# Performance work log

Hardware: AMD Instinct MI355X
Metric: run time of the kernel (lower is better)

Reference implementation:

```python
import jax, jax.numpy as jnp
import numpy as np

PI = float(np.pi)

def erp_xyz_coords(h, w):
    # matches calculate_erp_coord: pixel grid -> uv -> unit-sphere xyz
    yy, xx = jnp.meshgrid(jnp.linspace(0.0, h - 1.0, h), jnp.linspace(0.0, w - 1.0, w), indexing='ij')
    u = (xx - (w / 2.0 + 0.5)) / w * 2.0 * PI
    v = (yy - (h / 2.0 + 0.5)) / h * PI
    xyz = jnp.stack([jnp.cos(v) * jnp.sin(u), jnp.sin(v), jnp.cos(v) * jnp.cos(u)], axis=-1)
    return xyz.reshape(h * w, 3)  # (HW, 3)


def setup_inputs() -> dict:
    key = jax.random.key(0)
    ks = jax.random.split(key, 16)
    B, C, H, W = 1, 128, 16, 32
    Nkv = 1280
    s = 0.02
    inp = {
        'erp_feature': jax.random.normal(ks[0], (B, C, H, W), jnp.float32),
        'ico_feature': jax.random.normal(ks[1], (B, Nkv, C), jnp.float32),
        'ico_coord': jax.random.normal(ks[2], (B, Nkv, 3), jnp.float32),
        # SA branch params (torch Linear: y = x @ W.T + b, W is (out,in))
        'Wq_sa': jax.random.normal(ks[3], (C, C), jnp.float32) * s,
        'Wkv_sa': jax.random.normal(ks[4], (2 * C, C), jnp.float32) * s,
        'proj_sa_w': jax.random.normal(ks[5], (C, C), jnp.float32) * s,
        'proj_sa_b': jnp.zeros((C,), jnp.float32),
        # DA branch params
        'Wq_da': jax.random.normal(ks[6], (C, C), jnp.float32) * s,
        'Wkv_da': jax.random.normal(ks[7], (2 * C, C), jnp.float32) * s,
        'Wdelta': jax.random.normal(ks[8], (C, 3), jnp.float32) * s,
        'proj_da_w': jax.random.normal(ks[9], (C, C), jnp.float32) * s,
        'proj_da_b': jnp.zeros((C,), jnp.float32),
        # gates
        'gate_sa_w': jax.random.normal(ks[10], (C, 2 * C), jnp.float32) * s,
        'gate_da_w': jax.random.normal(ks[11], (C, 2 * C), jnp.float32) * s,
    }
    return inp


def _forward(erp_feature, ico_feature, ico_coord,
             Wq_sa, Wkv_sa, proj_sa_w, proj_sa_b,
             Wq_da, Wkv_da, Wdelta, proj_da_w, proj_da_b,
             gate_sa_w, gate_da_w):
    B, C, H, W = erp_feature.shape
    Nq = H * W
    q = erp_feature.reshape(B, C, Nq).transpose(0, 2, 1)  # (B, Nq, C)
    qc = erp_xyz_coords(H, W)[None]                        # (1, Nq, 3) broadcasts over B

    # ---- SA branch (iteration = 1) ----
    q_sa = q @ Wq_sa.T                                     # (B, Nq, C)
    kv_sa = (ico_feature @ Wkv_sa.T).reshape(B, -1, 2, C)
    k_sa, v_sa = kv_sa[:, :, 0], kv_sa[:, :, 1]
    attn_sa = jax.nn.softmax(jnp.einsum('bqc,bkc->bqk', q_sa, k_sa) * (C ** -0.5), axis=-1)
    out_sa = jnp.einsum('bqk,bkc->bqc', attn_sa, v_sa)
    # faithful to torch: .transpose(1,2).reshape(B, Nq, C) scrambles layout
    out_sa = out_sa.transpose(0, 2, 1).reshape(B, Nq, C)
    sa = out_sa @ proj_sa_w.T + proj_sa_b

    # ---- DA branch (iteration = 1) ----
    q_da = q @ Wq_da.T
    kv_da = (ico_feature @ Wkv_da.T).reshape(B, -1, 2, C)
    k_da, v_da = kv_da[:, :, 0], kv_da[:, :, 1]
    # feature affinity: sum_c exp(-|q_c - k_c|)   -> (B, Nq, Nkv)
    feat_aff = jnp.exp(-jnp.abs(q_da[:, :, None, :] - k_da[:, None, :, :])).sum(-1)
    # positional term: (exp(-|dq - dk|) @ Wdelta.T).sum(-1) == exp(...) . Wdelta.sum(0)
    pos_exp = jnp.exp(-jnp.abs(qc[:, :, None, :] - ico_coord[:, None, :, :]))  # (B,Nq,Nkv,3)
    pos_aff = jnp.einsum('bqkt,t->bqk', pos_exp, Wdelta.sum(0))
    attn_da = jax.nn.softmax((feat_aff + pos_aff) * (1.0 / C), axis=-1)
    out_da = jnp.einsum('bqk,bkc->bqc', attn_da, v_da)
    da = out_da @ proj_da_w.T + proj_da_b

    # ---- gated fusion ----
    cat = jnp.concatenate([sa, da], axis=-1)               # (B, Nq, 2C)
    sa_factor = jax.nn.sigmoid(cat @ gate_sa_w.T)
    da_factor = jax.nn.sigmoid(cat @ gate_da_w.T)
    fused = sa_factor * sa + da_factor * da                # (B, Nq, C)
    return fused.reshape(B, H, W, C).transpose(0, 3, 1, 2)  # (B, C, H, W)


def reference(erp_feature, ico_feature, ico_coord,
              Wq_sa, Wkv_sa, proj_sa_w, proj_sa_b,
              Wq_da, Wkv_da, Wdelta, proj_da_w, proj_da_b,
              gate_sa_w, gate_da_w):
    return _forward(erp_feature, ico_feature, ico_coord,
                    Wq_sa, Wkv_sa, proj_sa_w, proj_sa_b,
                    Wq_da, Wkv_da, Wdelta, proj_da_w, proj_da_b,
                    gate_sa_w, gate_da_w)
```

## Files before the change

### kernel.cpp

```cpp
#include <hip/hip_runtime.h>
#include <math.h>

#define NQ   512
#define NKV  1280
#define CDIM 128

#define OFF_WDSUM 0
#define OFF_SUMS  16
#define OFF_QSA   1056
#define OFF_QDA   66592
#define OFF_KSAT  132128
#define OFF_VSA   295968
#define OFF_KDAT  459808
#define OFF_VDA   623648
#define OFF_OUT   787488

__global__ __launch_bounds__(256) void prep_kernel(
    const float* __restrict__ erp, const float* __restrict__ ico,
    const float* __restrict__ wq_sa, const float* __restrict__ wq_da,
    const float* __restrict__ wkv_sa, const float* __restrict__ wkv_da,
    const float* __restrict__ wdelta, float* __restrict__ ws)
{
  int bx = blockIdx.x, t = threadIdx.x;
  if (bx < 320) {
    __shared__ float x4[4 * CDIM];
    int k0 = bx * 4;
    for (int i = t; i < 512; i += 256) {
      int ky = i >> 7, j = i & 127;
      x4[j * 4 + ky] = ico[(k0 + ky) * CDIM + j];
    }
    __syncthreads();
    const float4* wsa4 = (const float4*)(wkv_sa + t * CDIM);
    const float4* wda4 = (const float4*)(wkv_da + t * CDIM);
    float as0=0,as1=0,as2=0,as3=0, ad0=0,ad1=0,ad2=0,ad3=0;
    #pragma unroll 4
    for (int j4 = 0; j4 < 32; ++j4) {
      float4 wsv = wsa4[j4];
      float4 wdv = wda4[j4];
      float4 x0 = *(const float4*)&x4[(j4 * 4 + 0) * 4];
      float4 x1 = *(const float4*)&x4[(j4 * 4 + 1) * 4];
      float4 x2 = *(const float4*)&x4[(j4 * 4 + 2) * 4];
      float4 x3 = *(const float4*)&x4[(j4 * 4 + 3) * 4];
      as0 = fmaf(wsv.x, x0.x, as0); as1 = fmaf(wsv.x, x0.y, as1);
      as2 = fmaf(wsv.x, x0.z, as2); as3 = fmaf(wsv.x, x0.w, as3);
      ad0 = fmaf(wdv.x, x0.x, ad0); ad1 = fmaf(wdv.x, x0.y, ad1);
      ad2 = fmaf(wdv.x, x0.z, ad2); ad3 = fmaf(wdv.x, x0.w, ad3);
      as0 = fmaf(wsv.y, x1.x, as0); as1 = fmaf(wsv.y, x1.y, as1);
      as2 = fmaf(wsv.y, x1.z, as2); as3 = fmaf(wsv.y, x1.w, as3);
      ad0 = fmaf(wdv.y, x1.x, ad0); ad1 = fmaf(wdv.y, x1.y, ad1);
      ad2 = fmaf(wdv.y, x1.z, ad2); ad3 = fmaf(wdv.y, x1.w, ad3);
      as0 = fmaf(wsv.z, x2.x, as0); as1 = fmaf(wsv.z, x2.y, as1);
      as2 = fmaf(wsv.z, x2.z, as2); as3 = fmaf(wsv.z, x2.w, as3);
      ad0 = fmaf(wdv.z, x2.x, ad0); ad1 = fmaf(wdv.z, x2.y, ad1);
      ad2 = fmaf(wdv.z, x2.z, ad2); ad3 = fmaf(wdv.z, x2.w, ad3);
      as0 = fmaf(wsv.w, x3.x, as0); as1 = fmaf(wsv.w, x3.y, as1);
      as2 = fmaf(wsv.w, x3.z, as2); as3 = fmaf(wsv.w, x3.w, as3);
      ad0 = fmaf(wdv.w, x3.x, ad0); ad1 = fmaf(wdv.w, x3.y, ad1);
      ad2 = fmaf(wdv.w, x3.z, ad2); ad3 = fmaf(wdv.w, x3.w, ad3);
    }
    if (t < 128) {
      *(float4*)(ws + OFF_KSAT + t * NKV + k0) = make_float4(as0, as1, as2, as3);
      *(float4*)(ws + OFF_KDAT + t * NKV + k0) = make_float4(ad0, ad1, ad2, ad3);
    } else {
      int c = t - 128;
      ws[OFF_VSA + (k0 + 0) * CDIM + c] = as0;
      ws[OFF_VSA + (k0 + 1) * CDIM + c] = as1;
      ws[OFF_VSA + (k0 + 2) * CDIM + c] = as2;
      ws[OFF_VSA + (k0 + 3) * CDIM + c] = as3;
      ws[OFF_VDA + (k0 + 0) * CDIM + c] = ad0;
      ws[OFF_VDA + (k0 + 1) * CDIM + c] = ad1;
      ws[OFF_VDA + (k0 + 2) * CDIM + c] = ad2;
      ws[OFF_VDA + (k0 + 3) * CDIM + c] = ad3;
    }
  } else if (bx < 448) {
    __shared__ float q4[4 * CDIM];
    int n0 = (bx - 320) * 4;
    for (int i = t; i < 512; i += 256)
      q4[i] = erp[(i >> 2) * NQ + n0 + (i & 3)];
    __syncthreads();
    const float* w = (t < 128) ? wq_sa : wq_da;
    int c = t & 127;
    const float4* w4 = (const float4*)(w + c * CDIM);
    float a0 = 0.f, a1 = 0.f, a2 = 0.f, a3 = 0.f;
    #pragma unroll 8
    for (int j4 = 0; j4 < 32; ++j4) {
      float4 wv = w4[j4];
      float4 q0 = *(const float4*)&q4[(j4 * 4 + 0) * 4];
      float4 q1 = *(const float4*)&q4[(j4 * 4 + 1) * 4];
      float4 q2 = *(const float4*)&q4[(j4 * 4 + 2) * 4];
      float4 q3 = *(const float4*)&q4[(j4 * 4 + 3) * 4];
      a0 = fmaf(wv.x, q0.x, a0); a1 = fmaf(wv.x, q0.y, a1);
      a2 = fmaf(wv.x, q0.z, a2); a3 = fmaf(wv.x, q0.w, a3);
      a0 = fmaf(wv.y, q1.x, a0); a1 = fmaf(wv.y, q1.y, a1);
      a2 = fmaf(wv.y, q1.z, a2); a3 = fmaf(wv.y, q1.w, a3);
      a0 = fmaf(wv.z, q2.x, a0); a1 = fmaf(wv.z, q2.y, a1);
      a2 = fmaf(wv.z, q2.z, a2); a3 = fmaf(wv.z, q2.w, a3);
      a0 = fmaf(wv.w, q3.x, a0); a1 = fmaf(wv.w, q3.y, a1);
      a2 = fmaf(wv.w, q3.z, a2); a3 = fmaf(wv.w, q3.w, a3);
    }
    float* o = ws + ((t < 128) ? OFF_QSA : OFF_QDA);
    o[(n0 + 0) * CDIM + c] = a0;
    o[(n0 + 1) * CDIM + c] = a1;
    o[(n0 + 2) * CDIM + c] = a2;
    o[(n0 + 3) * CDIM + c] = a3;
  } else if (bx == 448) {
    *(float4*)(ws + OFF_SUMS + t * 4) = make_float4(0.f, 0.f, 0.f, 0.f);
    if (t < 3) {
      float s = 0.f;
      for (int i = 0; i < 128; ++i) s += wdelta[i * 3 + t];
      ws[OFF_WDSUM + t] = s;
    }
  } else {
    int base = OFF_OUT + (bx - 449) * 1024 + t * 4;
    *(float4*)(ws + base) = make_float4(0.f, 0.f, 0.f, 0.f);
  }
}

__global__ __launch_bounds__(256) void attn_kernel(
    const float* __restrict__ coord, float* __restrict__ ws)
{
  __shared__ __align__(16) float qjf[128][4];
  __shared__ __align__(16) float se[4][256];
  __shared__ float red[4][4];
  __shared__ float qcr[4][3];
  __shared__ float wdl[3];
  int b = blockIdx.x, t = threadIdx.x;
  int br = (b < 1280) ? 1 : 0;
  int n0, k0;
  if (br) { int g = b / 10;          n0 = g * 4; k0 = (b - g * 10) * 128; }
  else    { int bb = b - 1280, g = bb / 5; n0 = g * 4; k0 = (bb - g * 5) * 256; }

  const float* qsrc = ws + (br ? OFF_QDA : OFF_QSA);
  for (int i = t; i < 512; i += 256)
    qjf[i >> 2][i & 3] = qsrc[(n0 + (i & 3)) * CDIM + (i >> 2)];
  if (br) {
    if (t < 4) {
      int n = n0 + t;
      float x = (float)(n & 31), y = (float)(n >> 5);
      float u  = (x - 16.5f) * 0.19634954084936207f;
      float vv = (y -  8.5f) * 0.19634954084936207f;
      float cv = cosf(vv);
      qcr[t][0] = cv * sinf(u);
      qcr[t][1] = sinf(vv);
      qcr[t][2] = cv * cosf(u);
    }
    if (t >= 64 && t < 67) wdl[t - 64] = ws[OFF_WDSUM + (t - 64)];
  }
  __syncthreads();

  if (br) {
    int kl = t & 127, rp = t >> 7;
    int k = k0 + kl, rp2 = rp * 2;
    float c0 = coord[3 * k], c1 = coord[3 * k + 1], c2 = coord[3 * k + 2];
    float w0 = wdl[0], w1 = wdl[1], w2 = wdl[2];
    float pA = w0 * __expf(-fabsf(qcr[rp2][0] - c0))
             + w1 * __expf(-fabsf(qcr[rp2][1] - c1))
             + w2 * __expf(-fabsf(qcr[rp2][2] - c2));
    float pB = w0 * __expf(-fabsf(qcr[rp2 + 1][0] - c0))
             + w1 * __expf(-fabsf(qcr[rp2 + 1][1] - c1))
             + w2 * __expf(-fabsf(qcr[rp2 + 1][2] - c2));
    const float* kt = ws + OFF_KDAT + k;
    float accA = 0.f, accB = 0.f;
    for (int j8 = 0; j8 < 128; j8 += 8) {
      float kv0 = kt[(j8 + 0) * NKV];
      float kv1 = kt[(j8 + 1) * NKV];
      float kv2 = kt[(j8 + 2) * NKV];
      float kv3 = kt[(j8 + 3) * NKV];
      float kv4 = kt[(j8 + 4) * NKV];
      float kv5 = kt[(j8 + 5) * NKV];
      float kv6 = kt[(j8 + 6) * NKV];
      float kv7 = kt[(j8 + 7) * NKV];
      float2 q0 = *(const float2*)&qjf[j8 + 0][rp2];
      float2 q1 = *(const float2*)&qjf[j8 + 1][rp2];
      float2 q2 = *(const float2*)&qjf[j8 + 2][rp2];
      float2 q3 = *(const float2*)&qjf[j8 + 3][rp2];
      float2 q4 = *(const float2*)&qjf[j8 + 4][rp2];
      float2 q5 = *(const float2*)&qjf[j8 + 5][rp2];
      float2 q6 = *(const float2*)&qjf[j8 + 6][rp2];
      float2 q7 = *(const float2*)&qjf[j8 + 7][rp2];
      accA += __expf(-fabsf(q0.x - kv0)); accB += __expf(-fabsf(q0.y - kv0));
      accA += __expf(-fabsf(q1.x - kv1)); accB += __expf(-fabsf(q1.y - kv1));
      accA += __expf(-fabsf(q2.x - kv2)); accB += __expf(-fabsf(q2.y - kv2));
      accA += __expf(-fabsf(q3.x - kv3)); accB += __expf(-fabsf(q3.y - kv3));
      accA += __expf(-fabsf(q4.x - kv4)); accB += __expf(-fabsf(q4.y - kv4));
      accA += __expf(-fabsf(q5.x - kv5)); accB += __expf(-fabsf(q5.y - kv5));
      accA += __expf(-fabsf(q6.x - kv6)); accB += __expf(-fabsf(q6.y - kv6));
      accA += __expf(-fabsf(q7.x - kv7)); accB += __expf(-fabsf(q7.y - kv7));
    }
    const float i128 = 0.0078125f;
    float eA = __expf((accA + pA) * i128);
    float eB = __expf((accB + pB) * i128);
    se[rp2][kl]     = eA;
    se[rp2 + 1][kl] = eB;
    float sA = eA, sB = eB;
    #pragma unroll
    for (int o = 32; o > 0; o >>= 1) {
      sA += __shfl_down(sA, o, 64); sB += __shfl_down(sB, o, 64);
    }
    if ((t & 63) == 0) { int w = t >> 6; red[w][0] = sA; red[w][1] = sB; }
    __syncthreads();
    if (t < 4) {
      int base = 2 * (t >> 1);
      atomicAdd(ws + OFF_SUMS + 512 + n0 + t,
                red[base][t & 1] + red[base + 1][t & 1]);
    }
    int c = t & 127, h = t >> 7;
    int kb = h * 64;
    const float* vp = ws + OFF_VDA + (k0 + kb) * CDIM + c;
    float a0 = 0.f, a1 = 0.f, a2 = 0.f, a3 = 0.f;
    #pragma unroll 2
    for (int ko = 0; ko < 64; ko += 4) {
      int kk = kb + ko;
      float4 p0 = *(const float4*)&se[0][kk];
      float4 p1 = *(const float4*)&se[1][kk];
      float4 p2 = *(const float4*)&se[2][kk];
      float4 p3 = *(const float4*)&se[3][kk];
      float v0 = vp[(ko + 0) * CDIM];
      float v1 = vp[(ko + 1) * CDIM];
      float v2 = vp[(ko + 2) * CDIM];
      float v3 = vp[(ko + 3) * CDIM];
      a0 = fmaf(p0.x, v0, a0); a0 = fmaf(p0.y, v1, a0);
      a0 = fmaf(p0.z, v2, a0); a0 = fmaf(p0.w, v3, a0);
      a1 = fmaf(p1.x, v0, a1); a1 = fmaf(p1.y, v1, a1);
      a1 = fmaf(p1.z, v2, a1); a1 = fmaf(p1.w, v3, a1);
      a2 = fmaf(p2.x, v0, a2); a2 = fmaf(p2.y, v1, a2);
      a2 = fmaf(p2.z, v2, a2); a2 = fmaf(p2.w, v3, a2);
      a3 = fmaf(p3.x, v0, a3); a3 = fmaf(p3.y, v1, a3);
      a3 = fmaf(p3.z, v2, a3); a3 = fmaf(p3.w, v3, a3);
    }
    float* op = ws + OFF_OUT + NQ * CDIM + c;
    atomicAdd(op + (n0 + 0) * CDIM, a0);
    atomicAdd(op + (n0 + 1) * CDIM, a1);
    atomicAdd(op + (n0 + 2) * CDIM, a2);
    atomicAdd(op + (n0 + 3) * CDIM, a3);
  } else {
    const float* kt = ws + OFF_KSAT + k0 + t;
    float acc0 = 0.f, acc1 = 0.f, acc2 = 0.f, acc3 = 0.f;
    for (int j4 = 0; j4 < 128; j4 += 4) {
      float kv0 = kt[(j4 + 0) * NKV];
      float kv1 = kt[(j4 + 1) * NKV];
      float kv2 = kt[(j4 + 2) * NKV];
      float kv3 = kt[(j4 + 3) * NKV];
      float4 q0 = *(const float4*)qjf[j4 + 0];
      float4 q1 = *(const float4*)qjf[j4 + 1];
      float4 q2 = *(const float4*)qjf[j4 + 2];
      float4 q3 = *(const float4*)qjf[j4 + 3];
      acc0 = fmaf(q0.x, kv0, acc0); acc1 = fmaf(q0.y, kv0, acc1);
      acc2 = fmaf(q0.z, kv0, acc2); acc3 = fmaf(q0.w, kv0, acc3);
      acc0 = fmaf(q1.x, kv1, acc0); acc1 = fmaf(q1.y, kv1, acc1);
      acc2 = fmaf(q1.z, kv1, acc2); acc3 = fmaf(q1.w, kv1, acc3);
      acc0 = fmaf(q2.x, kv2, acc0); acc1 = fmaf(q2.y, kv2, acc1);
      acc2 = fmaf(q2.z, kv2, acc2); acc3 = fmaf(q2.w, kv2, acc3);
      acc0 = fmaf(q3.x, kv3, acc0); acc1 = fmaf(q3.y, kv3, acc1);
      acc2 = fmaf(q3.z, kv3, acc2); acc3 = fmaf(q3.w, kv3, acc3);
    }
    const float scl = 0.088388347648318447f;
    float e0 = __expf(acc0 * scl);
    float e1 = __expf(acc1 * scl);
    float e2 = __expf(acc2 * scl);
    float e3 = __expf(acc3 * scl);
    se[0][t] = e0; se[1][t] = e1; se[2][t] = e2; se[3][t] = e3;
    float s0 = e0, s1 = e1, s2 = e2, s3 = e3;
    #pragma unroll
    for (int o = 32; o > 0; o >>= 1) {
      s0 += __shfl_down(s0, o, 64); s1 += __shfl_down(s1, o, 64);
      s2 += __shfl_down(s2, o, 64); s3 += __shfl_down(s3, o, 64);
    }
    if ((t & 63) == 0) {
      int w = t >> 6;
      red[w][0] = s0; red[w][1] = s1; red[w][2] = s2; red[w][3] = s3;
    }
    __syncthreads();
    if (t < 4)
      atomicAdd(ws + OFF_SUMS + n0 + t,
                red[0][t] + red[1][t] + red[2][t] + red[3][t]);
    int c = t & 127, h = t >> 7;
    int kb = h * 128;
    const float* vp = ws + OFF_VSA + (k0 + kb) * CDIM + c;
    float a0 = 0.f, a1 = 0.f, a2 = 0.f, a3 = 0.f;
    #pragma unroll 2
    for (int ko = 0; ko < 128; ko += 4) {
      int kk = kb + ko;
      float4 p0 = *(const float4*)&se[0][kk];
      float4 p1 = *(const float4*)&se[1][kk];
      float4 p2 = *(const float4*)&se[2][kk];
      float4 p3 = *(const float4*)&se[3][kk];
      float v0 = vp[(ko + 0) * CDIM];
      float v1 = vp[(ko + 1) * CDIM];
      float v2 = vp[(ko + 2) * CDIM];
      float v3 = vp[(ko + 3) * CDIM];
      a0 = fmaf(p0.x, v0, a0); a0 = fmaf(p0.y, v1, a0);
      a0 = fmaf(p0.z, v2, a0); a0 = fmaf(p0.w, v3, a0);
      a1 = fmaf(p1.x, v0, a1); a1 = fmaf(p1.y, v1, a1);
      a1 = fmaf(p1.z, v2, a1); a1 = fmaf(p1.w, v3, a1);
      a2 = fmaf(p2.x, v0, a2); a2 = fmaf(p2.y, v1, a2);
      a2 = fmaf(p2.z, v2, a2); a2 = fmaf(p2.w, v3, a2);
      a3 = fmaf(p3.x, v0, a3); a3 = fmaf(p3.y, v1, a3);
      a3 = fmaf(p3.z, v2, a3); a3 = fmaf(p3.w, v3, a3);
    }
    float* op = ws + OFF_OUT + c;
    atomicAdd(op + (n0 + 0) * CDIM, a0);
    atomicAdd(op + (n0 + 1) * CDIM, a1);
    atomicAdd(op + (n0 + 2) * CDIM, a2);
    atomicAdd(op + (n0 + 3) * CDIM, a3);
  }
}

__global__ __launch_bounds__(256) void finalize_kernel(
    const float* __restrict__ psa, const float* __restrict__ bsa,
    const float* __restrict__ pda, const float* __restrict__ bda,
    const float* __restrict__ gsa, const float* __restrict__ gda,
    float* __restrict__ out, float* __restrict__ ws)
{
  __shared__ float sain[2][CDIM];
  __shared__ float dain[2][CDIM];
  __shared__ float cat[2][2 * CDIM];
  __shared__ float gl[2][2][CDIM];
  int i0 = blockIdx.x * 2, t = threadIdx.x;
  int h = t >> 7, c = t & 127;
  #pragma unroll
  for (int rr = 0; rr < 2; ++rr) {
    int i = i0 + rr;
    if (h == 0) {
      int row = (i & 3) * 128 + c;
      float s = ws[OFF_SUMS + row];
      sain[rr][c] = ws[OFF_OUT + row * CDIM + (i >> 2)] / s;
    } else {
      float s = ws[OFF_SUMS + 512 + i];
      dain[rr][c] = ws[OFF_OUT + NQ * CDIM + i * CDIM + c] / s;
    }
  }
  __syncthreads();
  {
    const float4* w4 = (const float4*)((h ? pda : psa) + c * CDIM);
    const float* in0 = h ? dain[0] : sain[0];
    const float* in1 = h ? dain[1] : sain[1];
    float a0 = 0, a1 = 0, b0 = 0, b1 = 0;
    #pragma unroll 8
    for (int j4 = 0; j4 < 32; ++j4) {
      float4 wv = w4[j4];
      float4 x0 = *(const float4*)&in0[j4 * 4];
      float4 x1 = *(const float4*)&in1[j4 * 4];
      a0 = fmaf(wv.x, x0.x, a0); a1 = fmaf(wv.y, x0.y, a1);
      a0 = fmaf(wv.z, x0.z, a0); a1 = fmaf(wv.w, x0.w, a1);
      b0 = fmaf(wv.x, x1.x, b0); b1 = fmaf(wv.y, x1.y, b1);
      b0 = fmaf(wv.z, x1.z, b0); b1 = fmaf(wv.w, x1.w, b1);
    }
    float bias = h ? bda[c] : bsa[c];
    cat[0][h * CDIM + c] = bias + a0 + a1;
    cat[1][h * CDIM + c] = bias + b0 + b1;
  }
  __syncthreads();
  {
    const float4* g4 = (const float4*)((h ? gda : gsa) + c * 2 * CDIM);
    float a0 = 0, a1 = 0, b0 = 0, b1 = 0;
    #pragma unroll 8
    for (int j4 = 0; j4 < 64; ++j4) {
      float4 gv = g4[j4];
      float4 c0 = *(const float4*)&cat[0][j4 * 4];
      float4 c1 = *(const float4*)&cat[1][j4 * 4];
      a0 = fmaf(gv.x, c0.x, a0); a1 = fmaf(gv.y, c0.y, a1);
      a0 = fmaf(gv.z, c0.z, a0); a1 = fmaf(gv.w, c0.w, a1);
      b0 = fmaf(gv.x, c1.x, b0); b1 = fmaf(gv.y, c1.y, b1);
      b0 = fmaf(gv.z, c1.z, b0); b1 = fmaf(gv.w, c1.w, b1);
    }
    gl[0][h][c] = 1.0f / (1.0f + __expf(-(a0 + a1)));
    gl[1][h][c] = 1.0f / (1.0f + __expf(-(b0 + b1)));
  }
  __syncthreads();
  {
    int i = i0 + h;
    out[c * NQ + i] = gl[h][0][c] * cat[h][c] + gl[h][1][c] * cat[h][CDIM + c];
  }
}

extern "C" void kernel_launch(void* const* d_in, const int* in_sizes, int n_in,
                              void* d_out, int out_size, void* d_ws, size_t ws_size,
                              hipStream_t stream)
{
  (void)in_sizes; (void)n_in; (void)out_size; (void)ws_size;
  const float* erp       = (const float*)d_in[0];
  const float* ico       = (const float*)d_in[1];
  const float* coord     = (const float*)d_in[2];
  const float* wq_sa     = (const float*)d_in[3];
  const float* wkv_sa    = (const float*)d_in[4];
  const float* proj_sa_w = (const float*)d_in[5];
  const float* proj_sa_b = (const float*)d_in[6];
  const float* wq_da     = (const float*)d_in[7];
  const float* wkv_da    = (const float*)d_in[8];
  const float* wdelta    = (const float*)d_in[9];
  const float* proj_da_w = (const float*)d_in[10];
  const float* proj_da_b = (const float*)d_in[11];
  const float* gate_sa   = (const float*)d_in[12];
  const float* gate_da   = (const float*)d_in[13];
  float* out = (float*)d_out;
  float* ws  = (float*)d_ws;

  hipLaunchKernelGGL(prep_kernel, dim3(577), dim3(256), 0, stream,
                     erp, ico, wq_sa, wq_da, wkv_sa, wkv_da, wdelta, ws);
  hipLaunchKernelGGL(attn_kernel, dim3(1920), dim3(256), 0, stream,
                     coord, ws);
  hipLaunchKernelGGL(finalize_kernel, dim3(256), dim3(256), 0, stream,
                     proj_sa_w, proj_sa_b, proj_da_w, proj_da_b,
                     gate_sa, gate_da, out, ws);
}
```

Measured before the change: 142.7 us.

## Prescale DA operands by log2e for exp2 and double-buffer K tiles in LDS

Q_da, K_da and the coordinates are premultiplied by log2(e) in the prep kernel, so the attention kernel can call the hardware exp2 directly instead of __expf, which multiplies by log2e on every call. The DA branch also stops reading strided K columns from global memory per thread. It now stages 16-row K chunks into a double-buffered LDS tile with coalesced float4 loads, prefetching the next chunk. This adds two block barriers per chunk and extra LDS use, which may reduce occupancy.

```diff
diff --git a/kernel.cpp b/kernel.cpp
--- a/kernel.cpp
+++ b/kernel.cpp
@@ -4,6 +4,9 @@
 #define NQ   512
 #define NKV  1280
 #define CDIM 128
+#define L2E  1.4426950408889634f
+
+__device__ __forceinline__ float fexp2(float x) { return __builtin_amdgcn_exp2f(x); }
 
 #define OFF_WDSUM 0
 #define OFF_SUMS  16
@@ -60,7 +63,8 @@
     }
     if (t < 128) {
       *(float4*)(ws + OFF_KSAT + t * NKV + k0) = make_float4(as0, as1, as2, as3);
-      *(float4*)(ws + OFF_KDAT + t * NKV + k0) = make_float4(ad0, ad1, ad2, ad3);
+      *(float4*)(ws + OFF_KDAT + t * NKV + k0) =
+          make_float4(ad0 * L2E, ad1 * L2E, ad2 * L2E, ad3 * L2E);
     } else {
       int c = t - 128;
       ws[OFF_VSA + (k0 + 0) * CDIM + c] = as0;
@@ -98,11 +102,12 @@
       a0 = fmaf(wv.w, q3.x, a0); a1 = fmaf(wv.w, q3.y, a1);
       a2 = fmaf(wv.w, q3.z, a2); a3 = fmaf(wv.w, q3.w, a3);
     }
+    float sc = (t < 128) ? 1.0f : L2E;
     float* o = ws + ((t < 128) ? OFF_QSA : OFF_QDA);
-    o[(n0 + 0) * CDIM + c] = a0;
-    o[(n0 + 1) * CDIM + c] = a1;
-    o[(n0 + 2) * CDIM + c] = a2;
-    o[(n0 + 3) * CDIM + c] = a3;
+    o[(n0 + 0) * CDIM + c] = a0 * sc;
+    o[(n0 + 1) * CDIM + c] = a1 * sc;
+    o[(n0 + 2) * CDIM + c] = a2 * sc;
+    o[(n0 + 3) * CDIM + c] = a3 * sc;
   } else if (bx == 448) {
     *(float4*)(ws + OFF_SUMS + t * 4) = make_float4(0.f, 0.f, 0.f, 0.f);
     if (t < 3) {
@@ -121,6 +126,7 @@
 {
   __shared__ __align__(16) float qjf[128][4];
   __shared__ __align__(16) float se[4][256];
+  __shared__ __align__(16) float kch[2][16][128];
   __shared__ float red[4][4];
   __shared__ float qcr[4][3];
   __shared__ float wdl[3];
@@ -140,9 +146,9 @@
       float u  = (x - 16.5f) * 0.19634954084936207f;
       float vv = (y -  8.5f) * 0.19634954084936207f;
       float cv = cosf(vv);
-      qcr[t][0] = cv * sinf(u);
-      qcr[t][1] = sinf(vv);
-      qcr[t][2] = cv * cosf(u);
+      qcr[t][0] = cv * sinf(u) * L2E;
+      qcr[t][1] = sinf(vv) * L2E;
+      qcr[t][2] = cv * cosf(u) * L2E;
     }
     if (t >= 64 && t < 67) wdl[t - 64] = ws[OFF_WDSUM + (t - 64)];
   }
@@ -151,45 +157,51 @@
   if (br) {
     int kl = t & 127, rp = t >> 7;
     int k = k0 + kl, rp2 = rp * 2;
-    float c0 = coord[3 * k], c1 = coord[3 * k + 1], c2 = coord[3 * k + 2];
+    float c0 = coord[3 * k]     * L2E;
+    float c1 = coord[3 * k + 1] * L2E;
+    float c2 = coord[3 * k + 2] * L2E;
     float w0 = wdl[0], w1 = wdl[1], w2 = wdl[2];
-    float pA = w0 * __expf(-fabsf(qcr[rp2][0] - c0))
-             + w1 * __expf(-fabsf(qcr[rp2][1] - c1))
-             + w2 * __expf(-fabsf(qcr[rp2][2] - c2));
-    float pB = w0 * __expf(-fabsf(qcr[rp2 + 1][0] - c0))
-             + w1 * __expf(-fabsf(qcr[rp2 + 1][1] - c1))
-             + w2 * __expf(-fabsf(qcr[rp2 + 1][2] - c2));
-    const float* kt = ws + OFF_KDAT + k;
+    float pA = w0 * fexp2(-fabsf(qcr[rp2][0] - c0))
+             + w1 * fexp2(-fabsf(qcr[rp2][1] - c1))
+             + w2 * fexp2(-fabsf(qcr[rp2][2] - c2));
+    float pB = w0 * fexp2(-fabsf(qcr[rp2 + 1][0] - c0))
+             + w1 * fexp2(-fabsf(qcr[rp2 + 1][1] - c1))
+             + w2 * fexp2(-fabsf(qcr[rp2 + 1][2] - c2));
+    const float* kbase = ws + OFF_KDAT + k0;
+    int srow = t >> 5;
+    int scol = (t & 31) * 4;
+    *(float4*)&kch[0][srow][scol] =
+        *(const float4*)(kbase + (srow) * NKV + scol);
+    *(float4*)&kch[0][srow + 8][scol] =
+        *(const float4*)(kbase + (srow + 8) * NKV + scol);
+    __syncthreads();
     float accA = 0.f, accB = 0.f;
-    for (int j8 = 0; j8 < 128; j8 += 8) {
-      float kv0 = kt[(j8 + 0) * NKV];
-      float kv1 = kt[(j8 + 1) * NKV];
-      float kv2 = kt[(j8 + 2) * NKV];
-      float kv3 = kt[(j8 + 3) * NKV];
-      float kv4 = kt[(j8 + 4) * NKV];
-      float kv5 = kt[(j8 + 5) * NKV];
-      float kv6 = kt[(j8 + 6) * NKV];
-      float kv7 = kt[(j8 + 7) * NKV];
-      float2 q0 = *(const float2*)&qjf[j8 + 0][rp2];
-      float2 q1 = *(const float2*)&qjf[j8 + 1][rp2];
-      float2 q2 = *(const float2*)&qjf[j8 + 2][rp2];
-      float2 q3 = *(const float2*)&qjf[j8 + 3][rp2];
-      float2 q4 = *(const float2*)&qjf[j8 + 4][rp2];
-      float2 q5 = *(const float2*)&qjf[j8 + 5][rp2];
-      float2 q6 = *(const float2*)&qjf[j8 + 6][rp2];
-      float2 q7 = *(const float2*)&qjf[j8 + 7][rp2];
-      accA += __expf(-fabsf(q0.x - kv0)); accB += __expf(-fabsf(q0.y - kv0));
-      accA += __expf(-fabsf(q1.x - kv1)); accB += __expf(-fabsf(q1.y - kv1));
-      accA += __expf(-fabsf(q2.x - kv2)); accB += __expf(-fabsf(q2.y - kv2));
-      accA += __expf(-fabsf(q3.x - kv3)); accB += __expf(-fabsf(q3.y - kv3));
-      accA += __expf(-fabsf(q4.x - kv4)); accB += __expf(-fabsf(q4.y - kv4));
-      accA += __expf(-fabsf(q5.x - kv5)); accB += __expf(-fabsf(q5.y - kv5));
-      accA += __expf(-fabsf(q6.x - kv6)); accB += __expf(-fabsf(q6.y - kv6));
-      accA += __expf(-fabsf(q7.x - kv7)); accB += __expf(-fabsf(q7.y - kv7));
-    }
-    const float i128 = 0.0078125f;
-    float eA = __expf((accA + pA) * i128);
-    float eB = __expf((accB + pB) * i128);
+    int cur = 0;
+    for (int jb = 0; jb < 128; jb += 16) {
+      float4 nx0, nx1;
+      bool more = (jb + 16) < 128;
+      if (more) {
+        nx0 = *(const float4*)(kbase + (jb + 16 + srow) * NKV + scol);
+        nx1 = *(const float4*)(kbase + (jb + 24 + srow) * NKV + scol);
+      }
+      #pragma unroll
+      for (int j2 = 0; j2 < 16; ++j2) {
+        float kv = kch[cur][j2][kl];
+        float2 q = *(const float2*)&qjf[jb + j2][rp2];
+        accA += fexp2(-fabsf(q.x - kv));
+        accB += fexp2(-fabsf(q.y - kv));
+      }
+      __syncthreads();
+      if (more) {
+        *(float4*)&kch[cur ^ 1][srow][scol]     = nx0;
+        *(float4*)&kch[cur ^ 1][srow + 8][scol] = nx1;
+      }
+      __syncthreads();
+      cur ^= 1;
+    }
+    const float lsc = 0.0078125f * L2E;
+    float eA = fexp2((accA + pA) * lsc);
+    float eB = fexp2((accB + pB) * lsc);
     se[rp2][kl]     = eA;
     se[rp2 + 1][kl] = eB;
     float sA = eA, sB = eB;
@@ -254,11 +266,11 @@
       acc0 = fmaf(q3.x, kv3, acc0); acc1 = fmaf(q3.y, kv3, acc1);
       acc2 = fmaf(q3.z, kv3, acc2); acc3 = fmaf(q3.w, kv3, acc3);
     }
-    const float scl = 0.088388347648318447f;
-    float e0 = __expf(acc0 * scl);
-    float e1 = __expf(acc1 * scl);
-    float e2 = __expf(acc2 * scl);
-    float e3 = __expf(acc3 * scl);
+    const float scl2 = 0.088388347648318447f * L2E;
+    float e0 = fexp2(acc0 * scl2);
+    float e1 = fexp2(acc1 * scl2);
+    float e2 = fexp2(acc2 * scl2);
+    float e3 = fexp2(acc3 * scl2);
     se[0][t] = e0; se[1][t] = e1; se[2][t] = e2; se[3][t] = e3;
     float s0 = e0, s1 = e1, s2 = e2, s3 = e3;
     #pragma unroll
```

After: 138.9 us, median of 2. 1.03x faster.
